# Kernel optimization log

Measured on AMD Instinct MI355X. Metric: run time of the kernel, lower is better.

The kernel has to match this reference:

```python
import jax, jax.numpy as jnp
import numpy as np
import math

HIDDEN = 1024
HEADS = 16
HEAD_DIM = HIDDEN // HEADS


def setup_inputs() -> dict:
    key = jax.random.key(0)
    ks = jax.random.split(key, 7)
    B, S = 2, 2048
    scale = 1.0 / math.sqrt(HIDDEN)
    return {
        "x": jax.random.normal(ks[0], (B, S, HIDDEN), dtype=jnp.float32),
        "Wq": jax.random.normal(ks[1], (HIDDEN, HIDDEN), dtype=jnp.float32) * scale,
        "Wk": jax.random.normal(ks[2], (HIDDEN, HIDDEN), dtype=jnp.float32) * scale,
        "Wv": jax.random.normal(ks[3], (HIDDEN, HIDDEN), dtype=jnp.float32) * scale,
        "Wo": jax.random.normal(ks[4], (HIDDEN, HIDDEN), dtype=jnp.float32) * scale,
        "quantum_phase": jax.random.normal(ks[5], (HEADS, HEAD_DIM), dtype=jnp.float32),
        "quantum_amplitude": jnp.ones((HEADS, HEAD_DIM), dtype=jnp.float32),
    }


def reference(x, Wq, Wk, Wv, Wo, quantum_phase, quantum_amplitude):
    B, S, d = x.shape
    H, D = HEADS, HEAD_DIM

    # per-head/per-channel quantum modulation: real(x*exp(i*phase)) == x*cos(phase)
    mod = (jnp.cos(quantum_phase) * quantum_amplitude)[None, :, None, :]  # [1,H,1,D]

    def proj(W):
        return (x @ W).reshape(B, S, H, D).transpose(0, 2, 1, 3)  # [B,H,S,D]

    q = proj(Wq) * mod
    k = proj(Wk) * mod
    v = proj(Wv) * mod

    scores = jnp.einsum("bhid,bhjd->bhij", q, k) / math.sqrt(D)  # [B,H,S,S]

    # quantum interference: scores[i,j] *= cos(2*pi*(i-j)/S)
    idx = jnp.arange(S, dtype=jnp.float32)
    cos_mat = jnp.cos(2.0 * math.pi * (idx[:, None] - idx[None, :]) / S)  # [S,S]
    scores = scores * cos_mat

    w = jax.nn.softmax(scores, axis=-1)
    # superposition of attention weights with key-rolled copy
    w = (w + jnp.roll(w, 1, axis=-1)) / math.sqrt(2.0)

    out = jnp.einsum("bhij,bhjd->bhid", w, v)  # [B,H,S,D]
    out = out.transpose(0, 2, 1, 3).reshape(B, S, d)
    return out @ Wo
```

## Files before the change

### kernel.cpp

```cpp
#include <hip/hip_runtime.h>
#include <hip/hip_bf16.h>
#include <math.h>

#define HIDDEN 1024
#define HEADS  16
#define HDIM   64
#define BATCH  2
#define SEQ    2048
#define ROWS   (BATCH*SEQ)
#define BH     (BATCH*HEADS)

typedef __attribute__((ext_vector_type(8))) short  short8;
typedef __attribute__((ext_vector_type(8))) __bf16 bf16x8;
typedef __attribute__((ext_vector_type(4))) float  f32x4;

static __device__ __forceinline__ unsigned short f2bf(float f) {
    unsigned int u = __builtin_bit_cast(unsigned int, f);
    u += 0x7FFFu + ((u >> 16) & 1u);
    return (unsigned short)(u >> 16);
}
static __device__ __forceinline__ float bf2f(unsigned short h) {
    unsigned int u = ((unsigned int)h) << 16;
    return __builtin_bit_cast(float, u);
}
static __device__ __forceinline__ f32x4 mfma16(short8 a, short8 b, f32x4 c) {
    return __builtin_amdgcn_mfma_f32_16x16x32_bf16(
        __builtin_bit_cast(bf16x8, a), __builtin_bit_cast(bf16x8, b), c, 0, 0, 0);
}
static __device__ __forceinline__ void gl_lds16(const unsigned short* g, unsigned short* l) {
    __builtin_amdgcn_global_load_lds(
        (const __attribute__((address_space(1))) unsigned int*)g,
        (__attribute__((address_space(3))) unsigned int*)l, 16, 0, 0);
}

__global__ void convert_x_kernel(const float* __restrict__ x, unsigned short* __restrict__ xb,
                                 const float* __restrict__ qp, const float* __restrict__ qa,
                                 float* __restrict__ mod, float* __restrict__ mod2,
                                 float* __restrict__ posc, float* __restrict__ poss) {
    int i = (blockIdx.x * 256 + threadIdx.x) * 4;
    float4 v = *(const float4*)(x + i);
    ushort4 o;
    o.x = f2bf(v.x); o.y = f2bf(v.y); o.z = f2bf(v.z); o.w = f2bf(v.w);
    *(ushort4*)(xb + i) = o;
    if (blockIdx.x < 8) {
        int k = blockIdx.x * 256 + threadIdx.x;
        if (k < HIDDEN) {
            float m = cosf(qp[k]) * qa[k];
            mod[k] = m;
            mod2[k] = m * m * 0.18033688011112042f;
        }
        if (k < SEQ) {
            float ang = (float)k * (6.283185307179586f / (float)SEQ);
            posc[k] = cosf(ang);
            poss[k] = sinf(ang);
        }
    }
}

__global__ __launch_bounds__(256) void transpose_w_kernel(
    const float* __restrict__ w0, const float* __restrict__ w1,
    const float* __restrict__ w2, const float* __restrict__ w3,
    unsigned short* __restrict__ wt) {
    __shared__ unsigned short tile[64][72];
    const float* src = (blockIdx.z == 0) ? w0 : (blockIdx.z == 1) ? w1 : (blockIdx.z == 2) ? w2 : w3;
    unsigned short* dst = wt + (size_t)blockIdx.z * HIDDEN * HIDDEN;
    int n0 = blockIdx.x * 64, k0 = blockIdx.y * 64;
    int t = threadIdx.x;
    int cg = t & 15, r0 = t >> 4;
#pragma unroll
    for (int rr = 0; rr < 4; rr++) {
        int kl = r0 + rr * 16;
        float4 v = *(const float4*)(src + (size_t)(k0 + kl) * HIDDEN + n0 + cg * 4);
        tile[cg*4+0][kl] = f2bf(v.x);
        tile[cg*4+1][kl] = f2bf(v.y);
        tile[cg*4+2][kl] = f2bf(v.z);
        tile[cg*4+3][kl] = f2bf(v.w);
    }
    __syncthreads();
#pragma unroll
    for (int rr = 0; rr < 4; rr++) {
        int nl = r0 + rr * 16;
        ushort4 o;
        o.x = tile[nl][cg*4+0]; o.y = tile[nl][cg*4+1];
        o.z = tile[nl][cg*4+2]; o.w = tile[nl][cg*4+3];
        *(ushort4*)(dst + (size_t)(n0 + nl) * HIDDEN + k0 + cg * 4) = o;
    }
}

__global__ __launch_bounds__(256) void gemm_kernel(
    const unsigned short* __restrict__ A, const unsigned short* __restrict__ WtBase,
    unsigned short* __restrict__ CBase, float* __restrict__ Out, int mode0) {
    __shared__ unsigned short Alds[128 * 64];
    __shared__ unsigned short Blds[128 * 64];
    const int mode = mode0 + blockIdx.z;
    const unsigned short* Bt = WtBase + (size_t)mode * HIDDEN * HIDDEN;
    unsigned short* Cout = CBase + (size_t)mode * ROWS * HIDDEN;
    const int m0 = blockIdx.x * 128, n0 = blockIdx.y * 128;
    const int tid = threadIdx.x;
    const int wave = tid >> 6, lane = tid & 63, quad = lane >> 4, l15 = lane & 15;
    const int wr = wave >> 1, wc = wave & 1;
    const int srow = lane >> 3;
    const int schunk = (lane & 7) ^ (srow & 7);

    f32x4 acc[4][4];
    const f32x4 z4 = {0.f, 0.f, 0.f, 0.f};
#pragma unroll
    for (int i = 0; i < 4; i++)
#pragma unroll
        for (int j = 0; j < 4; j++) acc[i][j] = z4;

    for (int k0 = 0; k0 < HIDDEN; k0 += 64) {
#pragma unroll
        for (int p = 0; p < 4; p++) {
            int rbase = p * 32 + wave * 8;
            gl_lds16(A  + (size_t)(m0 + rbase + srow) * HIDDEN + k0 + schunk * 8,
                     &Alds[rbase * 64]);
            gl_lds16(Bt + (size_t)(n0 + rbase + srow) * HIDDEN + k0 + schunk * 8,
                     &Blds[rbase * 64]);
        }
        __syncthreads();
        short8 aF[4][2], bF[4][2];
#pragma unroll
        for (int h = 0; h < 2; h++) {
#pragma unroll
            for (int i = 0; i < 4; i++) {
                int row = wr * 64 + i * 16 + l15;
                aF[i][h] = *(const short8*)(&Alds[row * 64 + ((h * 4 + quad) ^ (l15 & 7)) * 8]);
            }
#pragma unroll
            for (int j = 0; j < 4; j++) {
                int row = wc * 64 + j * 16 + l15;
                bF[j][h] = *(const short8*)(&Blds[row * 64 + ((h * 4 + quad) ^ (l15 & 7)) * 8]);
            }
        }
#pragma unroll
        for (int h = 0; h < 2; h++)
#pragma unroll
            for (int i = 0; i < 4; i++)
#pragma unroll
                for (int j = 0; j < 4; j++)
                    acc[i][j] = mfma16(aF[i][h], bF[j][h], acc[i][j]);
        __syncthreads();
    }

#pragma unroll
    for (int i = 0; i < 4; i++) {
        int mbase = m0 + wr * 64 + i * 16 + quad * 4;
#pragma unroll
        for (int j = 0; j < 4; j++) {
            int n = n0 + wc * 64 + j * 16 + l15;
#pragma unroll
            for (int r = 0; r < 4; r++) {
                float val = acc[i][j][r];
                int mm = mbase + r;
                if (mode == 3) Out[(size_t)mm * HIDDEN + n] = val;
                else           Cout[(size_t)mm * HIDDEN + n] = f2bf(val);
            }
        }
    }
}

__global__ __launch_bounds__(256) void vmod_shift(const unsigned short* __restrict__ Cv,
                                                  unsigned short* __restrict__ Vpt,
                                                  const float* __restrict__ mod) {
    __shared__ unsigned short lds[65][72];
    int bh = blockIdx.x, b = bh >> 4, h = bh & 15;
    int s0 = blockIdx.y * 64;
    int t = threadIdx.x;
    int cg = t & 15, r0 = t >> 4;
    const float4 m4 = *(const float4*)(mod + h * 64 + cg * 4);
#pragma unroll
    for (int rr = 0; rr < 4; rr++) {
        int row = r0 + rr * 16;
        ushort4 v = *(const ushort4*)(Cv + ((size_t)(b * SEQ + s0 + row)) * HIDDEN + h * 64 + cg * 4);
        lds[row][cg*4+0] = f2bf(bf2f(v.x) * m4.x);
        lds[row][cg*4+1] = f2bf(bf2f(v.y) * m4.y);
        lds[row][cg*4+2] = f2bf(bf2f(v.z) * m4.z);
        lds[row][cg*4+3] = f2bf(bf2f(v.w) * m4.w);
    }
    if (t < 16) {
        int srow = (s0 + 64) & (SEQ - 1);
        const float4 mm4 = *(const float4*)(mod + h * 64 + t * 4);
        ushort4 v = *(const ushort4*)(Cv + ((size_t)(b * SEQ + srow)) * HIDDEN + h * 64 + t * 4);
        lds[64][t*4+0] = f2bf(bf2f(v.x) * mm4.x);
        lds[64][t*4+1] = f2bf(bf2f(v.y) * mm4.y);
        lds[64][t*4+2] = f2bf(bf2f(v.z) * mm4.z);
        lds[64][t*4+3] = f2bf(bf2f(v.w) * mm4.w);
    }
    __syncthreads();
    int d = t & 63, sb = (t >> 6) * 16;
    unsigned short outv[16];
#pragma unroll
    for (int k = 0; k < 16; k++) {
        float a = bf2f(lds[sb + k][d]), bb = bf2f(lds[sb + k + 1][d]);
        outv[k] = f2bf((a + bb) * 0.7071067811865476f);
    }
    unsigned short* dst = Vpt + ((size_t)bh * 64 + d) * SEQ + s0 + sb;
#pragma unroll
    for (int k = 0; k < 16; k += 4) {
        ushort4 o; o.x = outv[k]; o.y = outv[k+1]; o.z = outv[k+2]; o.w = outv[k+3];
        *(ushort4*)(dst + k) = o;
    }
}

#define KT 64
#define PSTR 76
__global__ __launch_bounds__(256) void attn_kernel(const unsigned short* __restrict__ Cq,
                                                   const unsigned short* __restrict__ Ck,
                                                   const unsigned short* __restrict__ Vpt,
                                                   unsigned short* __restrict__ Ob,
                                                   const float* __restrict__ mod2,
                                                   const float* __restrict__ posc,
                                                   const float* __restrict__ poss) {
    __shared__ unsigned short Klds[2][KT * 64];
    __shared__ unsigned short Vtlds[2][64 * 64];
    __shared__ unsigned short Plds[4 * 32 * PSTR];
    const int bh = blockIdx.x;
    const int b = bh >> 4, h = bh & 15;
    const int tid = threadIdx.x, wave = tid >> 6, lane = tid & 63;
    const int quad = lane >> 4, l15 = lane & 15;
    const int q0 = blockIdx.y * 128 + wave * 32;

    short8 qf[2][2];
#pragma unroll
    for (int g = 0; g < 2; g++) {
        int ss = q0 + g * 16 + l15;
        const unsigned short* crow = Cq + ((size_t)(b * SEQ + ss)) * HIDDEN + h * 64;
#pragma unroll
        for (int kk = 0; kk < 2; kk++) {
            int bd = kk * 32 + quad * 8;
            short8 u = *(const short8*)(crow + bd);
            short8 q;
#pragma unroll
            for (int e = 0; e < 8; e++)
                q[e] = (short)f2bf(bf2f((unsigned short)u[e]) * mod2[h * 64 + bd + e]);
            qf[g][kk] = q;
        }
    }
    float ci[2][4], si[2][4];
#pragma unroll
    for (int g = 0; g < 2; g++)
#pragma unroll
        for (int r = 0; r < 4; r++) {
            int ss = q0 + g * 16 + quad * 4 + r;
            ci[g][r] = posc[ss];
            si[g][r] = poss[ss];
        }

    short8 ones;
#pragma unroll
    for (int e = 0; e < 8; e++) ones[e] = (short)0x3F80;

    const f32x4 z4 = {0.f, 0.f, 0.f, 0.f};
    f32x4 acc[2][4], accden[2];
#pragma unroll
    for (int g = 0; g < 2; g++) {
#pragma unroll
        for (int dt = 0; dt < 4; dt++) acc[g][dt] = z4;
        accden[g] = z4;
    }

    unsigned short* pw = &Plds[wave * 32 * PSTR];

    const unsigned short* Kbh = Ck  + ((size_t)b * SEQ) * HIDDEN + h * 64;
    const unsigned short* Vbh = Vpt + (size_t)bh * 64 * SEQ;

    auto stage = [&](int j, int buf) {
#pragma unroll
        for (int p = 0; p < 2; p++) {
            int rb = p * 32 + wave * 8;
            int r  = rb + (lane >> 3);
            int c  = (lane & 7) ^ (r & 7);
            gl_lds16(Kbh + (size_t)(j + r) * HIDDEN + c * 8, &Klds[buf][rb * 64]);
        }
#pragma unroll
        for (int p = 0; p < 2; p++) {
            int rb = p * 32 + wave * 8;
            int r  = rb + (lane >> 3);
            int c  = (lane & 7) ^ (r & 7);
            gl_lds16(Vbh + (size_t)r * SEQ + j + c * 8, &Vtlds[buf][rb * 64]);
        }
    };

    float cjc[4], sjc[4];
#pragma unroll
    for (int t2 = 0; t2 < 4; t2++) {
        int jj = t2 * 16 + l15;
        cjc[t2] = posc[jj]; sjc[t2] = poss[jj];
    }

    stage(0, 0);
    for (int it = 0; it < SEQ / KT; it++) {
        __syncthreads();
        float cjn[4] = {0.f, 0.f, 0.f, 0.f}, sjn[4] = {0.f, 0.f, 0.f, 0.f};
        if (it + 1 < SEQ / KT) {
            stage((it + 1) * KT, (it + 1) & 1);
#pragma unroll
            for (int t2 = 0; t2 < 4; t2++) {
                int jj = (it + 1) * KT + t2 * 16 + l15;
                cjn[t2] = posc[jj]; sjn[t2] = poss[jj];
            }
        }
        const int buf = it & 1;

#pragma unroll
        for (int t2 = 0; t2 < 4; t2++) {
            float cj = cjc[t2], sj = sjc[t2];
            f32x4 sc[2] = {z4, z4};
#pragma unroll
            for (int kk = 0; kk < 2; kk++) {
                int ch = (kk * 4 + quad) ^ (l15 & 7);
                short8 kf = *(const short8*)(&Klds[buf][(t2 * 16 + l15) * 64 + ch * 8]);
#pragma unroll
                for (int g = 0; g < 2; g++)
                    sc[g] = mfma16(qf[g][kk], kf, sc[g]);
            }
#pragma unroll
            for (int g = 0; g < 2; g++) {
#pragma unroll
                for (int r = 0; r < 4; r++) {
                    float w = ci[g][r] * cj + si[g][r] * sj;
                    float p = __builtin_amdgcn_exp2f(sc[g][r] * w);
                    unsigned short pt = (unsigned short)(__builtin_bit_cast(unsigned int, p) >> 16);
                    pw[(g * 16 + quad * 4 + r) * PSTR + t2 * 16 + l15] = pt;
                }
            }
        }

#pragma unroll
        for (int pt = 0; pt < 2; pt++) {
            short8 pa0 = *(const short8*)(&pw[(l15) * PSTR + pt * 32 + quad * 8]);
            short8 pa1 = *(const short8*)(&pw[(16 + l15) * PSTR + pt * 32 + quad * 8]);
            accden[0] = mfma16(pa0, ones, accden[0]);
            accden[1] = mfma16(pa1, ones, accden[1]);
#pragma unroll
            for (int dt = 0; dt < 4; dt++) {
                int ch = (pt * 4 + quad) ^ (l15 & 7);
                short8 vb = *(const short8*)(&Vtlds[buf][(dt * 16 + l15) * 64 + ch * 8]);
                acc[0][dt] = mfma16(pa0, vb, acc[0][dt]);
                acc[1][dt] = mfma16(pa1, vb, acc[1][dt]);
            }
        }
#pragma unroll
        for (int t2 = 0; t2 < 4; t2++) { cjc[t2] = cjn[t2]; sjc[t2] = sjn[t2]; }
    }

#pragma unroll
    for (int g = 0; g < 2; g++) {
        float rinv[4];
#pragma unroll
        for (int r = 0; r < 4; r++) rinv[r] = 1.0f / accden[g][r];
#pragma unroll
        for (int dt = 0; dt < 4; dt++) {
#pragma unroll
            for (int r = 0; r < 4; r++) {
                int q = q0 + g * 16 + quad * 4 + r;
                int d = dt * 16 + l15;
                Ob[((size_t)(b * SEQ + q)) * HIDDEN + h * 64 + d] = f2bf(acc[g][dt][r] * rinv[r]);
            }
        }
    }
}

extern "C" void kernel_launch(void* const* d_in, const int* in_sizes, int n_in,
                              void* d_out, int out_size, void* d_ws, size_t ws_size,
                              hipStream_t stream) {
    const float* x  = (const float*)d_in[0];
    const float* Wq = (const float*)d_in[1];
    const float* Wk = (const float*)d_in[2];
    const float* Wv = (const float*)d_in[3];
    const float* Wo = (const float*)d_in[4];
    const float* qp = (const float*)d_in[5];
    const float* qa = (const float*)d_in[6];
    char* ws = (char*)d_ws;

    unsigned short* Xb  = (unsigned short*)(ws);
    unsigned short* Wt  = (unsigned short*)(ws + (size_t)( 8 << 20));
    unsigned short* Cq  = (unsigned short*)(ws + (size_t)(16 << 20));
    unsigned short* Ck  = (unsigned short*)(ws + (size_t)(24 << 20));
    unsigned short* Cv  = (unsigned short*)(ws + (size_t)(32 << 20));
    unsigned short* Vpt = (unsigned short*)(ws + (size_t)(40 << 20));
    float* mod  = (float*)(ws + (size_t)(48 << 20));
    float* mod2 = mod + 1024;
    float* posc = mod2 + 1024;
    float* poss = posc + 2048;
    float* out  = (float*)d_out;

    convert_x_kernel<<<4096, 256, 0, stream>>>(x, Xb, qp, qa, mod, mod2, posc, poss);
    transpose_w_kernel<<<dim3(16, 16, 4), 256, 0, stream>>>(Wq, Wk, Wv, Wo, Wt);
    gemm_kernel<<<dim3(32, 8, 3), 256, 0, stream>>>(Xb, Wt, Cq, out, 0);
    vmod_shift<<<dim3(32, 32), 256, 0, stream>>>(Cv, Vpt, mod);
    attn_kernel<<<dim3(32, 16), 256, 0, stream>>>(Cq, Ck, Vpt, Xb , mod2, posc, poss);
    gemm_kernel<<<dim3(32, 8, 1), 256, 0, stream>>>(Xb, Wt, Cq, out, 3);
}
```

Before: 254.3 us.

## Double-buffer GEMM LDS with smaller 64x128 tiles and K=32 steps

The projection GEMM now uses a 64x128 output tile with a K-step of 32 and two LDS buffers. The next K-slice is loaded while the current one is computed, so only one barrier per iteration is needed. The grid doubles in x, giving more workgroups to fill the CUs (the output-projection GEMM previously had only 256 blocks). In exchange each block reuses data less and runs more loop iterations with fewer MFMAs per barrier.

```diff
diff --git a/kernel.cpp b/kernel.cpp
--- a/kernel.cpp
+++ b/kernel.cpp
@@ -90,62 +90,62 @@
 __global__ __launch_bounds__(256) void gemm_kernel(
     const unsigned short* __restrict__ A, const unsigned short* __restrict__ WtBase,
     unsigned short* __restrict__ CBase, float* __restrict__ Out, int mode0) {
-    __shared__ unsigned short Alds[128 * 64];
-    __shared__ unsigned short Blds[128 * 64];
+    __shared__ unsigned short Alds[2][64 * 32];
+    __shared__ unsigned short Blds[2][128 * 32];
     const int mode = mode0 + blockIdx.z;
     const unsigned short* Bt = WtBase + (size_t)mode * HIDDEN * HIDDEN;
     unsigned short* Cout = CBase + (size_t)mode * ROWS * HIDDEN;
-    const int m0 = blockIdx.x * 128, n0 = blockIdx.y * 128;
+    const int m0 = blockIdx.x * 64, n0 = blockIdx.y * 128;
     const int tid = threadIdx.x;
     const int wave = tid >> 6, lane = tid & 63, quad = lane >> 4, l15 = lane & 15;
     const int wr = wave >> 1, wc = wave & 1;
-    const int srow = lane >> 3;
-    const int schunk = (lane & 7) ^ (srow & 7);
-
-    f32x4 acc[4][4];
+    const int srow4 = lane >> 2;
+    const int schunk = (lane & 3) ^ (srow4 & 3);
+    const int rchunk = quad ^ (l15 & 3);
+
+    f32x4 acc[2][4];
     const f32x4 z4 = {0.f, 0.f, 0.f, 0.f};
 #pragma unroll
-    for (int i = 0; i < 4; i++)
+    for (int i = 0; i < 2; i++)
 #pragma unroll
         for (int j = 0; j < 4; j++) acc[i][j] = z4;
 
-    for (int k0 = 0; k0 < HIDDEN; k0 += 64) {
-#pragma unroll
-        for (int p = 0; p < 4; p++) {
-            int rbase = p * 32 + wave * 8;
-            gl_lds16(A  + (size_t)(m0 + rbase + srow) * HIDDEN + k0 + schunk * 8,
-                     &Alds[rbase * 64]);
-            gl_lds16(Bt + (size_t)(n0 + rbase + srow) * HIDDEN + k0 + schunk * 8,
-                     &Blds[rbase * 64]);
-        }
+    auto stage = [&](int k0, int buf) {
+        {
+            int rb = wave * 16;
+            gl_lds16(A + (size_t)(m0 + rb + srow4) * HIDDEN + k0 + schunk * 8,
+                     &Alds[buf][rb * 32]);
+        }
+#pragma unroll
+        for (int p = 0; p < 2; p++) {
+            int rb = p * 64 + wave * 16;
+            gl_lds16(Bt + (size_t)(n0 + rb + srow4) * HIDDEN + k0 + schunk * 8,
+                     &Blds[buf][rb * 32]);
+        }
+    };
+
+    stage(0, 0);
+    for (int it = 0; it < HIDDEN / 32; it++) {
         __syncthreads();
-        short8 aF[4][2], bF[4][2];
-#pragma unroll
-        for (int h = 0; h < 2; h++) {
-#pragma unroll
-            for (int i = 0; i < 4; i++) {
-                int row = wr * 64 + i * 16 + l15;
-                aF[i][h] = *(const short8*)(&Alds[row * 64 + ((h * 4 + quad) ^ (l15 & 7)) * 8]);
-            }
-#pragma unroll
-            for (int j = 0; j < 4; j++) {
-                int row = wc * 64 + j * 16 + l15;
-                bF[j][h] = *(const short8*)(&Blds[row * 64 + ((h * 4 + quad) ^ (l15 & 7)) * 8]);
-            }
-        }
-#pragma unroll
-        for (int h = 0; h < 2; h++)
-#pragma unroll
-            for (int i = 0; i < 4; i++)
-#pragma unroll
-                for (int j = 0; j < 4; j++)
-                    acc[i][j] = mfma16(aF[i][h], bF[j][h], acc[i][j]);
-        __syncthreads();
-    }
-
-#pragma unroll
-    for (int i = 0; i < 4; i++) {
-        int mbase = m0 + wr * 64 + i * 16 + quad * 4;
+        if (it + 1 < HIDDEN / 32) stage((it + 1) * 32, (it + 1) & 1);
+        const int buf = it & 1;
+        short8 aF[2], bF[4];
+#pragma unroll
+        for (int i = 0; i < 2; i++)
+            aF[i] = *(const short8*)(&Alds[buf][(wr * 32 + i * 16 + l15) * 32 + rchunk * 8]);
+#pragma unroll
+        for (int j = 0; j < 4; j++)
+            bF[j] = *(const short8*)(&Blds[buf][(wc * 64 + j * 16 + l15) * 32 + rchunk * 8]);
+#pragma unroll
+        for (int i = 0; i < 2; i++)
+#pragma unroll
+            for (int j = 0; j < 4; j++)
+                acc[i][j] = mfma16(aF[i], bF[j], acc[i][j]);
+    }
+
+#pragma unroll
+    for (int i = 0; i < 2; i++) {
+        int mbase = m0 + wr * 32 + i * 16 + quad * 4;
 #pragma unroll
         for (int j = 0; j < 4; j++) {
             int n = n0 + wc * 64 + j * 16 + l15;
@@ -388,8 +388,8 @@
 
     convert_x_kernel<<<4096, 256, 0, stream>>>(x, Xb, qp, qa, mod, mod2, posc, poss);
     transpose_w_kernel<<<dim3(16, 16, 4), 256, 0, stream>>>(Wq, Wk, Wv, Wo, Wt);
-    gemm_kernel<<<dim3(32, 8, 3), 256, 0, stream>>>(Xb, Wt, Cq, out, 0);
+    gemm_kernel<<<dim3(64, 8, 3), 256, 0, stream>>>(Xb, Wt, Cq, out, 0);
     vmod_shift<<<dim3(32, 32), 256, 0, stream>>>(Cv, Vpt, mod);
     attn_kernel<<<dim3(32, 16), 256, 0, stream>>>(Cq, Ck, Vpt, Xb , mod2, posc, poss);
-    gemm_kernel<<<dim3(32, 8, 1), 256, 0, stream>>>(Xb, Wt, Cq, out, 3);
-}
+    gemm_kernel<<<dim3(64, 8, 1), 256, 0, stream>>>(Xb, Wt, Cq, out, 3);
+}
```

Measured after the change: 260.9 us. 1.03x slower.
